# Performance work log

Measured on AMD Instinct MI355X. Metric: run time of the kernel, lower is better.

## Reference

```python
import jax, jax.numpy as jnp
import numpy as np

LMAX = 2; C = 64; H = 8; D = C // H
N_NODES = 10000; N_EDGES = 160000
M = (LMAX + 1) ** 2                      # 9 spherical components
RAD_IN = 64; RAD_HID = 64
WNUM = (LMAX + 1) * C                    # per-edge CP-TP weights: one per (l, channel)
L_OF_M = jnp.array([l for l in range(LMAX + 1) for _ in range(2 * l + 1)])
LN_EPS = 1e-5


def _lin(x, W, b=None):
    # Linear over channel (last) dim; bias applied ONLY to scalar (m=0) component
    y = jnp.einsum('nmc,cd->nmd', x, W)
    if b is not None:
        y = y.at[:, 0, :].add(b)
    return y


def _cp_tp(x, sh, w_lc):
    # CP tensor product with SH: channelwise product, per-(l, channel) radial weight
    # x: [E, M, C], sh: [E, M], w_lc: [E, LMAX+1, C]
    return x * sh[:, :, None] * w_lc[:, L_OF_M, :]


def _radial(s, W1, b1, g, b, W2, off):
    h = s @ W1 + b1
    mu = h.mean(-1, keepdims=True)
    var = h.var(-1, keepdims=True)
    h = (h - mu) / jnp.sqrt(var + LN_EPS) * g + b
    h = jax.nn.silu(h)
    return (h @ W2 + off).reshape(-1, LMAX + 1, C)


def _smooth_lrelu(x, a=0.2):
    return (1 + a) / 2 * x + (1 - a) / 2 * x * (2 * jax.nn.sigmoid(x) - 1)


def _gate(x):
    c = x.shape[-1] // 2
    v = x[..., :c]
    g = jax.nn.sigmoid(x[:, 0, c:])[:, None, :]
    return jnp.concatenate([jax.nn.silu(v[:, :1, :]), v[:, 1:, :] * g], axis=1)


def _seg_softmax(a, idx, n):
    # numerically stable softmax over edges grouped by destination node
    m = jax.ops.segment_max(a, idx, num_segments=n)
    e = jnp.exp(a - m[idx])
    s = jax.ops.segment_sum(e, idx, num_segments=n)
    return e / (s[idx] + 1e-16)


def setup_inputs():
    key = jax.random.key(0)
    ks = jax.random.split(key, 16)
    def w(k, shape, fan_in):
        return jax.random.normal(k, shape, jnp.float32) / np.sqrt(fan_in)
    bound = 1.0 / np.sqrt(RAD_HID)
    return {
        'node_input': jax.random.normal(ks[0], (N_NODES, M, C), jnp.float32),
        'edge_attr': jax.random.normal(ks[1], (N_EDGES, M), jnp.float32),
        'edge_scalars': jax.random.normal(ks[2], (N_EDGES, RAD_IN), jnp.float32),
        'W_src': w(ks[3], (C, C), C), 'b_src': jnp.zeros((C,), jnp.float32),
        'W_dst': w(ks[4], (C, C), C),
        'rad_W1': w(ks[5], (RAD_IN, RAD_HID), RAD_IN),
        'rad_b1': jnp.zeros((RAD_HID,), jnp.float32),
        'rad_ln_g': jnp.ones((RAD_HID,), jnp.float32),
        'rad_ln_b': jnp.zeros((RAD_HID,), jnp.float32),
        'rad_W2': w(ks[6], (RAD_HID, WNUM), RAD_HID),
        'rad_offset': jax.random.uniform(ks[7], (WNUM,), jnp.float32, -bound, bound),
        'W_alpha': w(ks[8], (C, C), C), 'b_alpha': jnp.zeros((C,), jnp.float32),
        'alpha_dot': w(ks[9], (H, D), D),
        'W_value': w(ks[10], (C, 2 * C), C), 'b_value': jnp.zeros((2 * C,), jnp.float32),
        'W_proj': w(ks[11], (C, C), C), 'b_proj': jnp.zeros((C,), jnp.float32),
        'edge_src': jax.random.randint(ks[12], (N_EDGES,), 0, N_NODES),
        'edge_dst': jax.random.randint(ks[13], (N_EDGES,), 0, N_NODES),
        'batch': jnp.zeros((N_NODES,), jnp.int32),
    }


def reference(node_input, edge_attr, edge_scalars, W_src, b_src, W_dst,
              rad_W1, rad_b1, rad_ln_g, rad_ln_b, rad_W2, rad_offset,
              W_alpha, b_alpha, alpha_dot, W_value, b_value, W_proj, b_proj,
              edge_src, edge_dst, batch):
    # gather: per-edge merged message [E, M, C]
    msg = _lin(node_input, W_src, b_src)[edge_src] + _lin(node_input, W_dst)[edge_dst]
    # per-edge radial weights for both tensor products [E, LMAX+1, C]
    w_lc = _radial(edge_scalars, rad_W1, rad_b1, rad_ln_g, rad_ln_b, rad_W2, rad_offset)
    msg = _cp_tp(msg, edge_attr, w_lc)
    # alpha path: scalar channel only
    alpha = _lin(msg, W_alpha, b_alpha)[:, 0, :].reshape(-1, H, D)
    alpha = _smooth_lrelu(alpha)[:, None]                 # [E, 1, H, D]
    alpha = jnp.einsum('bikd,kd->bik', alpha, alpha_dot)  # [E, 1, H]
    alpha = _seg_softmax(alpha, edge_dst, N_NODES)        # dropout disabled (eval)
    # value path
    value = _gate(_lin(msg, W_value, b_value))
    value = _cp_tp(value, edge_attr, w_lc)
    value = value.reshape(N_EDGES, M, H, D)
    # scatter-aggregate to destination nodes
    out = jax.ops.segment_sum(value * alpha[:, :, :, None], edge_dst, num_segments=N_NODES)
    return _lin(out.reshape(N_NODES, M, C), W_proj, b_proj)
```

## Files before the change

kernel.cpp:

```cpp
#include <hip/hip_runtime.h>
#include <stdint.h>

#define NN 10000
#define NE 160000

struct BF16 { unsigned short v; };
typedef _Float16 h2_t __attribute__((ext_vector_type(2)));
typedef _Float16 f16x8 __attribute__((ext_vector_type(8)));
typedef float f32x4 __attribute__((ext_vector_type(4)));

__device__ __forceinline__ float cvt(float x) { return x; }
__device__ __forceinline__ float cvt(BF16 x) {
    union { unsigned int i; float f; } u; u.i = ((unsigned int)x.v) << 16; return u.f;
}
__device__ __forceinline__ unsigned short f2b_us(float f) {
    union { float f; unsigned int i; } v; v.f = f;
    unsigned int x = v.i;
    unsigned int lsb = (x >> 16) & 1u;
    x += 0x7fffu + lsb;
    return (unsigned short)(x >> 16);
}
__device__ __forceinline__ float rlane(float v, int l) {
    return __uint_as_float((unsigned int)__builtin_amdgcn_readlane(__float_as_uint(v), l));
}
__device__ __forceinline__ h2_t rlane_pk(h2_t v, int l) {
    union { h2_t h; unsigned int u; } c; c.h = v;
    c.u = (unsigned int)__builtin_amdgcn_readlane(c.u, l);
    return c.h;
}
__device__ __forceinline__ h2_t pkh2(float a, float b) {
    h2_t r; r[0] = (_Float16)a; r[1] = (_Float16)b; return r;
}
__device__ __forceinline__ float fdot2f(h2_t a, h2_t b, float c) {
#if __has_builtin(__builtin_amdgcn_fdot2)
    return __builtin_amdgcn_fdot2(a, b, c, false);
#else
    return fmaf((float)a[0], (float)b[0], fmaf((float)a[1], (float)b[1], c));
#endif
}
__device__ __forceinline__ float sigm(float x) { return 1.0f / (1.0f + __expf(-x)); }
__device__ __forceinline__ int clampi(int v, int hi) { return (unsigned)v >= (unsigned)hi ? 0 : v; }

__device__ __forceinline__ void stOut(float* p, size_t i, float v) { p[i] = v; }
__device__ __forceinline__ void stOut(unsigned short* p, size_t i, float v) { p[i] = f2b_us(v); }

__device__ __forceinline__ unsigned okey(float f) {
    unsigned b = __float_as_uint(f);
    return (b & 0x80000000u) ? ~b : (b | 0x80000000u);
}
__device__ __forceinline__ float okdec(unsigned k) {
    unsigned b = (k & 0x80000000u) ? (k ^ 0x80000000u) : ~k;
    return __uint_as_float(b);
}

__device__ __forceinline__ f16x8 ld8f16(const BF16* p) {
    uint4 v = *(const uint4*)p;
    unsigned w0 = v.x, w1 = v.y, w2 = v.z, w3 = v.w;
    f16x8 r;
    union { unsigned u; float f; } c;
    c.u = (w0 & 0xFFFFu) << 16;  r[0] = (_Float16)c.f;
    c.u = (w0 & 0xFFFF0000u);    r[1] = (_Float16)c.f;
    c.u = (w1 & 0xFFFFu) << 16;  r[2] = (_Float16)c.f;
    c.u = (w1 & 0xFFFF0000u);    r[3] = (_Float16)c.f;
    c.u = (w2 & 0xFFFFu) << 16;  r[4] = (_Float16)c.f;
    c.u = (w2 & 0xFFFF0000u);    r[5] = (_Float16)c.f;
    c.u = (w3 & 0xFFFFu) << 16;  r[6] = (_Float16)c.f;
    c.u = (w3 & 0xFFFF0000u);    r[7] = (_Float16)c.f;
    return r;
}
__device__ __forceinline__ f16x8 ld8f16(const float* p) {
    float4 a = *(const float4*)p;
    float4 b = *(const float4*)(p + 4);
    f16x8 r;
    r[0] = (_Float16)a.x; r[1] = (_Float16)a.y; r[2] = (_Float16)a.z; r[3] = (_Float16)a.w;
    r[4] = (_Float16)b.x; r[5] = (_Float16)b.y; r[6] = (_Float16)b.z; r[7] = (_Float16)b.w;
    return r;
}

__global__ void k0_zero(int* __restrict__ cnt, int* __restrict__ csr, int* __restrict__ flag,
                        float* __restrict__ nsum, unsigned* __restrict__ mseg,
                        float* __restrict__ sseg, const unsigned short* __restrict__ x) {
    int i = blockIdx.x * blockDim.x + threadIdx.x;
    if (blockIdx.x == 0) {
        __shared__ int sbad[256];
        int bad = 0;
        for (int j = threadIdx.x; j < 16384; j += blockDim.x) {
            unsigned e = (x[j] >> 7) & 0xFFu;
            bad += (e == 0xFFu);
        }
        sbad[threadIdx.x] = bad;
        __syncthreads();
        for (int o = 128; o >= 1; o >>= 1) {
            if (threadIdx.x < o) sbad[threadIdx.x] += sbad[threadIdx.x + o];
            __syncthreads();
        }
        if (threadIdx.x == 0) *flag = (sbad[0] > 0) ? 0 : 1;
    }
    if (i < NN) cnt[i] = 0;
    if (i < NE) csr[i] = 0;
    if (i < NN * 8) { mseg[i] = 0u; sseg[i] = 0.f; }
    for (int j = i; j < NN * 576; j += gridDim.x * blockDim.x) nsum[j] = 0.f;
}

template<typename T>
__device__ void k1m_body(const T* x, const T* Ws, const T* bs, const T* Wd,
                         _Float16* fs, _Float16* fd, _Float16 (*Yt)[128])
{
    const int lane = threadIdx.x & 63;
    const int c16 = lane & 15;
    const int kg  = lane >> 4;

    f16x8 bWs[4][2], bWd[4][2];
#pragma unroll
    for (int t = 0; t < 4; t++)
#pragma unroll
        for (int kh = 0; kh < 2; kh++) {
            f16x8 f1, f2;
#pragma unroll
            for (int j = 0; j < 8; j++) {
                int k = kh * 32 + kg * 8 + j;
                f1[j] = (_Float16)cvt(Ws[(size_t)k * 64 + t * 16 + c16]);
                f2[j] = (_Float16)cvt(Wd[(size_t)k * 64 + t * 16 + c16]);
            }
            bWs[t][kh] = f1; bWd[t][kh] = f2;
        }
    float bsv[4];
#pragma unroll
    for (int t = 0; t < 4; t++) bsv[t] = cvt(bs[t * 16 + c16]);

    const int NT = (NN * 9) / 16;
    for (int tile = blockIdx.x * 4 + (threadIdx.x >> 6); tile < NT; tile += gridDim.x * 4) {
        const int r0 = tile * 16;
        f16x8 a0 = ld8f16(&x[(size_t)(r0 + c16) * 64 + kg * 8]);
        f16x8 a1 = ld8f16(&x[(size_t)(r0 + c16) * 64 + 32 + kg * 8]);
        f32x4 hs[4] = {{0,0,0,0},{0,0,0,0},{0,0,0,0},{0,0,0,0}};
        f32x4 hd[4] = {{0,0,0,0},{0,0,0,0},{0,0,0,0},{0,0,0,0}};
#pragma unroll
        for (int t = 0; t < 4; t++) {
            hs[t] = __builtin_amdgcn_mfma_f32_16x16x32_f16(a0, bWs[t][0], hs[t], 0, 0, 0);
            hs[t] = __builtin_amdgcn_mfma_f32_16x16x32_f16(a1, bWs[t][1], hs[t], 0, 0, 0);
            hd[t] = __builtin_amdgcn_mfma_f32_16x16x32_f16(a0, bWd[t][0], hd[t], 0, 0, 0);
            hd[t] = __builtin_amdgcn_mfma_f32_16x16x32_f16(a1, bWd[t][1], hd[t], 0, 0, 0);
        }
#pragma unroll
        for (int t = 0; t < 4; t++)
#pragma unroll
            for (int r = 0; r < 4; r++) {
                int row = kg * 4 + r;
                float vs = hs[t][r];
                if (((r0 + row) % 9) == 0) vs += bsv[t];
                Yt[row][t * 16 + c16] = (_Float16)vs;
                Yt[row][64 + t * 16 + c16] = (_Float16)hd[t][r];
            }
#pragma unroll
        for (int j = 0; j < 2; j++) {
            int c = lane + 64 * j;
            int row = c >> 3;
            int cc = (c & 7) * 8;
            *(f16x8*)&fs[(size_t)(r0 + row) * 64 + cc] = *(const f16x8*)&Yt[row][cc];
            *(f16x8*)&fd[(size_t)(r0 + row) * 64 + cc] = *(const f16x8*)&Yt[row][64 + cc];
        }
    }
}

__global__ __launch_bounds__(256) void k1m_feats(
    const void* x, const void* Ws, const void* bs, const void* Wd,
    _Float16* fs, _Float16* fd, const int* flag)
{
    __shared__ _Float16 Y[4][16][128];
    const int wv = threadIdx.x >> 6;
    if (*flag) k1m_body<BF16>((const BF16*)x, (const BF16*)Ws, (const BF16*)bs, (const BF16*)Wd,
                              fs, fd, Y[wv]);
    else       k1m_body<float>((const float*)x, (const float*)Ws, (const float*)bs, (const float*)Wd,
                               fs, fd, Y[wv]);
}

__global__ void k2a_count(const int* __restrict__ dst, int* __restrict__ cnt) {
    for (int e = blockIdx.x * blockDim.x + threadIdx.x; e < NE; e += gridDim.x * blockDim.x)
        atomicAdd(&cnt[clampi(dst[e], NN)], 1);
}

__global__ __launch_bounds__(1024) void k2b_scan(const int* __restrict__ cnt,
                                                 int* __restrict__ off, int* __restrict__ cur) {
    __shared__ int part[1024];
    int t = threadIdx.x;
    int base = t * 10;
    int loc[10]; int s = 0;
#pragma unroll
    for (int k = 0; k < 10; k++) { int i = base + k; int v = (i < NN) ? cnt[i] : 0; loc[k] = v; s += v; }
    part[t] = s; __syncthreads();
    for (int o = 1; o < 1024; o <<= 1) {
        int v = (t >= o) ? part[t - o] : 0;
        __syncthreads();
        part[t] += v;
        __syncthreads();
    }
    int run = (t == 0) ? 0 : part[t - 1];
#pragma unroll
    for (int k = 0; k < 10; k++) {
        int i = base + k;
        if (i < NN) { off[i] = run; cur[i] = run; run += loc[k]; }
    }
    if (t == 1023) off[NN] = part[1023];
}

__global__ void k2c_fill(const int* __restrict__ dst, int* __restrict__ cur, int* __restrict__ csr) {
    for (int e = blockIdx.x * blockDim.x + threadIdx.x; e < NE; e += gridDim.x * blockDim.x) {
        int d = clampi(dst[e], NN);
        int p = atomicAdd(&cur[d], 1);
        if ((unsigned)p < (unsigned)NE) csr[p] = e;
    }
}

template<typename T>
__device__ void k3m_body(const T* es, const T* W1, const T* b1g, const T* gg, const T* bbv,
                         const T* W2, const T* roff, _Float16* wlc,
                         _Float16 (*Yt)[200])
{
    const int lane = threadIdx.x & 63;
    const int c16 = lane & 15;
    const int kg  = lane >> 4;

    f16x8 bW1[4][2], bW2[12][2];
#pragma unroll
    for (int t = 0; t < 4; t++)
#pragma unroll
        for (int kh = 0; kh < 2; kh++) {
            f16x8 f;
#pragma unroll
            for (int j = 0; j < 8; j++) {
                int k = kh * 32 + kg * 8 + j;
                f[j] = (_Float16)cvt(W1[(size_t)k * 64 + t * 16 + c16]);
            }
            bW1[t][kh] = f;
        }
#pragma unroll
    for (int t = 0; t < 12; t++)
#pragma unroll
        for (int kh = 0; kh < 2; kh++) {
            f16x8 f;
#pragma unroll
            for (int j = 0; j < 8; j++) {
                int k = kh * 32 + kg * 8 + j;
                f[j] = (_Float16)cvt(W2[(size_t)k * 192 + t * 16 + c16]);
            }
            bW2[t][kh] = f;
        }
    float b1v[4], gv[4], bv[4], rv[12];
#pragma unroll
    for (int t = 0; t < 4; t++) {
        b1v[t] = cvt(b1g[t * 16 + c16]);
        gv[t]  = cvt(gg[t * 16 + c16]);
        bv[t]  = cvt(bbv[t * 16 + c16]);
    }
#pragma unroll
    for (int t = 0; t < 12; t++) rv[t] = cvt(roff[t * 16 + c16]);

    const int NT = NE / 16;
    for (int tile = blockIdx.x * 4 + (threadIdx.x >> 6); tile < NT; tile += gridDim.x * 4) {
        const int e0 = tile * 16;
        f16x8 a0 = ld8f16(&es[(size_t)(e0 + c16) * 64 + kg * 8]);
        f16x8 a1 = ld8f16(&es[(size_t)(e0 + c16) * 64 + 32 + kg * 8]);
        f32x4 h[4] = {{0,0,0,0},{0,0,0,0},{0,0,0,0},{0,0,0,0}};
#pragma unroll
        for (int t = 0; t < 4; t++) {
            h[t] = __builtin_amdgcn_mfma_f32_16x16x32_f16(a0, bW1[t][0], h[t], 0, 0, 0);
            h[t] = __builtin_amdgcn_mfma_f32_16x16x32_f16(a1, bW1[t][1], h[t], 0, 0, 0);
        }
#pragma unroll
        for (int r = 0; r < 4; r++) {
            float x0 = h[0][r] + b1v[0], x1 = h[1][r] + b1v[1];
            float x2 = h[2][r] + b1v[2], x3 = h[3][r] + b1v[3];
            float s = x0 + x1 + x2 + x3;
            float q = x0 * x0 + x1 * x1 + x2 * x2 + x3 * x3;
            s += __shfl_xor(s, 1, 64); q += __shfl_xor(q, 1, 64);
            s += __shfl_xor(s, 2, 64); q += __shfl_xor(q, 2, 64);
            s += __shfl_xor(s, 4, 64); q += __shfl_xor(q, 4, 64);
            s += __shfl_xor(s, 8, 64); q += __shfl_xor(q, 8, 64);
            float mu = s * (1.0f / 64.0f);
            float var = fmaxf(q * (1.0f / 64.0f) - mu * mu, 0.0f);
            float rs = rsqrtf(var + 1e-5f);
            int row = kg * 4 + r;
#pragma unroll
            for (int t = 0; t < 4; t++) {
                float xt = (t == 0) ? x0 : (t == 1) ? x1 : (t == 2) ? x2 : x3;
                float v = (xt - mu) * rs * gv[t] + bv[t];
                v = v * sigm(v);
                Yt[row][t * 16 + c16] = (_Float16)v;
            }
        }
        f16x8 a20 = *(const f16x8*)&Yt[c16][kg * 8];
        f16x8 a21 = *(const f16x8*)&Yt[c16][32 + kg * 8];
        f32x4 y[12] = {{0,0,0,0},{0,0,0,0},{0,0,0,0},{0,0,0,0},{0,0,0,0},{0,0,0,0},
                       {0,0,0,0},{0,0,0,0},{0,0,0,0},{0,0,0,0},{0,0,0,0},{0,0,0,0}};
#pragma unroll
        for (int t = 0; t < 12; t++) {
            y[t] = __builtin_amdgcn_mfma_f32_16x16x32_f16(a20, bW2[t][0], y[t], 0, 0, 0);
            y[t] = __builtin_amdgcn_mfma_f32_16x16x32_f16(a21, bW2[t][1], y[t], 0, 0, 0);
        }
#pragma unroll
        for (int t = 0; t < 12; t++)
#pragma unroll
            for (int r = 0; r < 4; r++)
                Yt[kg * 4 + r][t * 16 + c16] = (_Float16)(y[t][r] + rv[t]);
#pragma unroll
        for (int j = 0; j < 6; j++) {
            int c = lane + 64 * j;
            int row = c / 24;
            int cc = (c % 24) * 8;
            *(f16x8*)&wlc[(size_t)(e0 + row) * 192 + cc] = *(const f16x8*)&Yt[row][cc];
        }
    }
}

__global__ __launch_bounds__(256) void k3m_wlc(
    const void* es, const void* W1, const void* b1, const void* g, const void* bln,
    const void* W2, const void* roff, _Float16* wlc, const int* flag)
{
    __shared__ _Float16 Y[4][16][200];
    const int wv = threadIdx.x >> 6;
    if (*flag) k3m_body<BF16>((const BF16*)es, (const BF16*)W1, (const BF16*)b1, (const BF16*)g,
                              (const BF16*)bln, (const BF16*)W2, (const BF16*)roff, wlc, Y[wv]);
    else       k3m_body<float>((const float*)es, (const float*)W1, (const float*)b1, (const float*)g,
                               (const float*)bln, (const float*)W2, (const float*)roff, wlc, Y[wv]);
}

template<typename T>
__device__ void k4m_body(const T* ea, const _Float16* fs, const _Float16* fd,
                         const _Float16* wlc, const T* Wa, const T* ba, const T* adot,
                         const int* esrc, const int* edst, float* alpha, unsigned* mseg,
                         float (*aS)[8])
{
    const int lane = threadIdx.x & 63;
    const int c16 = lane & 15;
    const int kgr = lane >> 4;

    f16x8 bWa[4][2];
#pragma unroll
    for (int t = 0; t < 4; t++)
#pragma unroll
        for (int kh = 0; kh < 2; kh++) {
            f16x8 f;
#pragma unroll
            for (int j = 0; j < 8; j++) {
                int k = kh * 32 + kgr * 8 + j;
                f[j] = (_Float16)cvt(Wa[(size_t)k * 64 + t * 16 + c16]);
            }
            bWa[t][kh] = f;
        }
    float bav[4], adv[4];
#pragma unroll
    for (int t = 0; t < 4; t++) {
        bav[t] = cvt(ba[t * 16 + c16]);
        adv[t] = cvt(adot[t * 16 + c16]);
    }

    const int NT = NE / 16;
    for (int tile = blockIdx.x * 4 + (threadIdx.x >> 6); tile < NT; tile += gridDim.x * 4) {
        const int e0 = tile * 16;
        const int eA = e0 + c16;
        const int sn = clampi(esrc[eA], NN);
        const int dn = clampi(edst[eA], NN);
        f16x8 fs0 = *(const f16x8*)&fs[(size_t)sn * 576 + kgr * 8];
        f16x8 fs1 = *(const f16x8*)&fs[(size_t)sn * 576 + 32 + kgr * 8];
        f16x8 fd0 = *(const f16x8*)&fd[(size_t)dn * 576 + kgr * 8];
        f16x8 fd1 = *(const f16x8*)&fd[(size_t)dn * 576 + 32 + kgr * 8];
        f16x8 wl0 = *(const f16x8*)&wlc[(size_t)eA * 192 + kgr * 8];
        f16x8 wl1 = *(const f16x8*)&wlc[(size_t)eA * 192 + 32 + kgr * 8];
        _Float16 eh = (_Float16)cvt(ea[(size_t)eA * 9]);
        f16x8 ev;
#pragma unroll
        for (int j = 0; j < 8; j++) ev[j] = eh;
        f16x8 a0 = (fs0 + fd0) * ev * wl0;
        f16x8 a1 = (fs1 + fd1) * ev * wl1;

        f32x4 d[4] = {{0,0,0,0},{0,0,0,0},{0,0,0,0},{0,0,0,0}};
#pragma unroll
        for (int t = 0; t < 4; t++) {
            d[t] = __builtin_amdgcn_mfma_f32_16x16x32_f16(a0, bWa[t][0], d[t], 0, 0, 0);
            d[t] = __builtin_amdgcn_mfma_f32_16x16x32_f16(a1, bWa[t][1], d[t], 0, 0, 0);
        }
#pragma unroll
        for (int t = 0; t < 4; t++)
#pragma unroll
            for (int r = 0; r < 4; r++) {
                float aw = d[t][r] + bav[t];
                float f = aw * (0.2f + 0.8f * sigm(aw));
                float p = f * adv[t];
                p += __shfl_xor(p, 1, 64);
                p += __shfl_xor(p, 2, 64);
                p += __shfl_xor(p, 4, 64);
                if ((c16 & 7) == 0)
                    aS[kgr * 4 + r][t * 2 + (c16 >> 3)] = p;
            }
#pragma unroll
        for (int j = 0; j < 2; j++) {
            int idx = lane * 2 + j;
            int row = idx >> 3, h = idx & 7;
            float p = aS[row][h];
            alpha[(size_t)(e0 + row) * 8 + h] = p;
            int dnr = clampi(edst[e0 + row], NN);
            atomicMax(&mseg[dnr * 8 + h], okey(p));
        }
    }
}

__global__ __launch_bounds__(256) void k4m_alpha(
    const void* ea, const _Float16* fs, const _Float16* fd, const _Float16* wlc,
    const void* Wa, const void* ba, const void* adot,
    const int* esrc, const int* edst, float* alpha, unsigned* mseg, const int* flag)
{
    __shared__ float A[4][16][8];
    const int wv = threadIdx.x >> 6;
    if (*flag) k4m_body<BF16>((const BF16*)ea, fs, fd, wlc, (const BF16*)Wa, (const BF16*)ba,
                              (const BF16*)adot, esrc, edst, alpha, mseg, A[wv]);
    else       k4m_body<float>((const float*)ea, fs, fd, wlc, (const float*)Wa, (const float*)ba,
                               (const float*)adot, esrc, edst, alpha, mseg, A[wv]);
}

__global__ void k5b_expsum(const int* __restrict__ edst, const unsigned* __restrict__ mseg,
                           float* __restrict__ alpha, float* __restrict__ sseg) {
    int t = blockIdx.x * blockDim.x + threadIdx.x;
    if (t >= NE * 8) return;
    int e = t >> 3, h = t & 7;
    int dn = clampi(edst[e], NN);
    float m = okdec(mseg[dn * 8 + h]);
    float ex = __expf(alpha[t] - m);
    alpha[t] = ex;
    unsafeAtomicAdd(&sseg[dn * 8 + h], ex);
}

template<typename T>
__device__ void k6m_body(const int* off, const int* csr, const int* esrc,
                         const T* ea, const _Float16* fs, const _Float16* fd,
                         const _Float16* wlc, const T* Wv, const T* bv,
                         const float* alpha, const float* sseg, float* nsum,
                         _Float16 (*wlS)[16][72], float (*mtS)[20])
{
    const int lane = threadIdx.x & 63;
    const int wvid = threadIdx.x >> 6;
    const int c16 = lane & 15;
    const int kg  = lane >> 4;

    const int gw0  = blockIdx.x * 4 + wvid;
    const int half = gw0 & 1;

    f16x8 bfV[2][2], bfG[2][2];
    float bvv[2], bgv[2];
    int colg[2], hh[2];
#pragma unroll
    for (int t = 0; t < 2; t++) {
        colg[t] = (half * 2 + t) * 16 + c16;
        hh[t] = colg[t] >> 3;
#pragma unroll
        for (int kh = 0; kh < 2; kh++) {
            f16x8 b8v, b8g;
#pragma unroll
            for (int j = 0; j < 8; j++) {
                int k = kh * 32 + kg * 8 + j;
                b8v[j] = (_Float16)cvt(Wv[(size_t)k * 128 + colg[t]]);
                b8g[j] = (_Float16)cvt(Wv[(size_t)k * 128 + 64 + colg[t]]);
            }
            bfV[t][kh] = b8v; bfG[t][kh] = b8g;
        }
        bvv[t] = cvt(bv[colg[t]]);
        bgv[t] = cvt(bv[64 + colg[t]]);
    }

    for (int gw = gw0; gw < NN * 2; gw += gridDim.x * 4) {
        const int n = gw >> 1;
        const int b = off[n], e_end = off[n + 1];
        if (b >= e_end) continue;

        float invs[2];
        invs[0] = 1.0f / (sseg[n * 8 + hh[0]] + 1e-16f);
        invs[1] = 1.0f / (sseg[n * 8 + hh[1]] + 1e-16f);

        const size_t fdb = (size_t)n * 576;
        const size_t nbase = (size_t)n * 576;

        for (int p0 = b; p0 < e_end; p0 += 16) {
            int pA = p0 + c16; if (pA >= e_end) pA = e_end - 1;
            const int eA = clampi(csr[pA], NE);
            const int snA = clampi(esrc[eA], NN);
            const size_t fsb = (size_t)snA * 576;
            const size_t wlb = (size_t)eA * 192;

#pragma unroll
            for (int l = 0; l < 3; l++)
#pragma unroll
                for (int kh = 0; kh < 2; kh++)
                    *(f16x8*)&wlS[l][c16][kh * 32 + kg * 8] =
                        *(const f16x8*)&wlc[wlb + (size_t)l * 64 + kh * 32 + kg * 8];
            float eao[9];
#pragma unroll
            for (int m = 0; m < 9; m++) eao[m] = cvt(ea[(size_t)eA * 9 + m]);
            if (kg == 0) {
#pragma unroll
                for (int m = 0; m < 9; m++) mtS[c16][m] = eao[m];
            }
            mtS[c16][10 + kg * 2]     = alpha[(size_t)eA * 8 + kg * 2];
            mtS[c16][10 + kg * 2 + 1] = alpha[(size_t)eA * 8 + kg * 2 + 1];

            float awm[2][4];
#pragma unroll
            for (int r = 0; r < 4; r++) {
                int row = kg * 4 + r;
                float vm = (p0 + row < e_end) ? 1.f : 0.f;
#pragma unroll
                for (int t = 0; t < 2; t++)
                    awm[t][r] = mtS[row][10 + hh[t]] * invs[t] * vm;
            }

            float gtv[2][4];
            {
                f16x8 a0, a1;
                {
                    f16x8 w0 = *(const f16x8*)&wlS[0][c16][kg * 8];
                    f16x8 w1 = *(const f16x8*)&wlS[0][c16][32 + kg * 8];
                    f16x8 fd0 = *(const f16x8*)&fd[fdb + kg * 8];
                    f16x8 fd1 = *(const f16x8*)&fd[fdb + 32 + kg * 8];
                    f16x8 fs0 = *(const f16x8*)&fs[fsb + kg * 8];
                    f16x8 fs1 = *(const f16x8*)&fs[fsb + 32 + kg * 8];
                    _Float16 eh = (_Float16)eao[0];
                    f16x8 ev;
#pragma unroll
                    for (int j = 0; j < 8; j++) ev[j] = eh;
                    a0 = (fs0 + fd0) * ev * w0;
                    a1 = (fs1 + fd1) * ev * w1;
                }
                f32x4 d[2] = {{0,0,0,0},{0,0,0,0}};
                f32x4 g[2] = {{0,0,0,0},{0,0,0,0}};
#pragma unroll
                for (int t = 0; t < 2; t++) {
                    d[t] = __builtin_amdgcn_mfma_f32_16x16x32_f16(a0, bfV[t][0], d[t], 0, 0, 0);
                    d[t] = __builtin_amdgcn_mfma_f32_16x16x32_f16(a1, bfV[t][1], d[t], 0, 0, 0);
                    g[t] = __builtin_amdgcn_mfma_f32_16x16x32_f16(a0, bfG[t][0], g[t], 0, 0, 0);
                    g[t] = __builtin_amdgcn_mfma_f32_16x16x32_f16(a1, bfG[t][1], g[t], 0, 0, 0);
                }
#pragma unroll
                for (int t = 0; t < 2; t++) {
                    float ps = 0.f;
#pragma unroll
                    for (int r = 0; r < 4; r++) {
                        int row = kg * 4 + r;
                        gtv[t][r] = sigm(g[t][r] + bgv[t]);
                        float v = d[t][r] + bvv[t];
                        float f = v * sigm(v);
                        float wlv = (float)wlS[0][row][colg[t]];
                        float eam = mtS[row][0];
                        ps = fmaf(f * (eam * wlv), awm[t][r], ps);
                    }
                    ps += __shfl_xor(ps, 16, 64);
                    ps += __shfl_xor(ps, 32, 64);
                    if (kg == 0) unsafeAtomicAdd(&nsum[nbase + colg[t]], ps);
                }
            }
#pragma unroll 2
            for (int m = 1; m < 9; m++) {
                const int l = (m < 4) ? 1 : 2;
                f16x8 a0, a1;
                {
                    const size_t mo = (size_t)m * 64;
                    f16x8 w0 = *(const f16x8*)&wlS[l][c16][kg * 8];
                    f16x8 w1 = *(const f16x8*)&wlS[l][c16][32 + kg * 8];
                    f16x8 fd0 = *(const f16x8*)&fd[fdb + mo + kg * 8];
                    f16x8 fd1 = *(const f16x8*)&fd[fdb + mo + 32 + kg * 8];
                    f16x8 fs0 = *(const f16x8*)&fs[fsb + mo + kg * 8];
                    f16x8 fs1 = *(const f16x8*)&fs[fsb + mo + 32 + kg * 8];
                    _Float16 eh = (_Float16)eao[m];
                    f16x8 ev;
#pragma unroll
                    for (int j = 0; j < 8; j++) ev[j] = eh;
                    a0 = (fs0 + fd0) * ev * w0;
                    a1 = (fs1 + fd1) * ev * w1;
                }
                f32x4 d[2] = {{0,0,0,0},{0,0,0,0}};
#pragma unroll
                for (int t = 0; t < 2; t++) {
                    d[t] = __builtin_amdgcn_mfma_f32_16x16x32_f16(a0, bfV[t][0], d[t], 0, 0, 0);
                    d[t] = __builtin_amdgcn_mfma_f32_16x16x32_f16(a1, bfV[t][1], d[t], 0, 0, 0);
                }
#pragma unroll
                for (int t = 0; t < 2; t++) {
                    float ps = 0.f;
#pragma unroll
                    for (int r = 0; r < 4; r++) {
                        int row = kg * 4 + r;
                        float f = d[t][r] * gtv[t][r];
                        float wlv = (float)wlS[l][row][colg[t]];
                        float eam = mtS[row][m];
                        ps = fmaf(f * (eam * wlv), awm[t][r], ps);
                    }
                    ps += __shfl_xor(ps, 16, 64);
                    ps += __shfl_xor(ps, 32, 64);
                    if (kg == 0) unsafeAtomicAdd(&nsum[nbase + (size_t)m * 64 + colg[t]], ps);
                }
            }
        }
    }
}

__global__ __launch_bounds__(256) void k6m_fused(
    const int* off, const int* csr, const int* esrc,
    const void* ea, const _Float16* fs, const _Float16* fd, const _Float16* wlc,
    const void* Wv, const void* bv,
    const float* alpha, const float* sseg, float* nsum, const int* flag)
{
    __shared__ _Float16 shwl[4][3][16][72];
    __shared__ float    shmt[4][16][20];
    const int wvid = threadIdx.x >> 6;
    if (*flag) k6m_body<BF16>(off, csr, esrc, (const BF16*)ea, fs, fd, wlc,
                              (const BF16*)Wv, (const BF16*)bv, alpha, sseg, nsum,
                              shwl[wvid], shmt[wvid]);
    else       k6m_body<float>(off, csr, esrc, (const float*)ea, fs, fd, wlc,
                               (const float*)Wv, (const float*)bv, alpha, sseg, nsum,
                               shwl[wvid], shmt[wvid]);
}

template<typename T, typename OT>
__device__ void k7m_body(const float* ns, const T* Wp, const T* bp, OT* out, OT (*Yt)[72])
{
    const int lane = threadIdx.x & 63;
    const int c16 = lane & 15;
    const int kg  = lane >> 4;

    f16x8 bWp[4][2];
#pragma unroll
    for (int t = 0; t < 4; t++)
#pragma unroll
        for (int kh = 0; kh < 2; kh++) {
            f16x8 f;
#pragma unroll
            for (int j = 0; j < 8; j++) {
                int k = kh * 32 + kg * 8 + j;
                f[j] = (_Float16)cvt(Wp[(size_t)k * 64 + t * 16 + c16]);
            }
            bWp[t][kh] = f;
        }
    float bpv[4];
#pragma unroll
    for (int t = 0; t < 4; t++) bpv[t] = cvt(bp[t * 16 + c16]);

    const int NT = (NN * 9) / 16;
    for (int tile = blockIdx.x * 4 + (threadIdx.x >> 6); tile < NT; tile += gridDim.x * 4) {
        const int r0 = tile * 16;
        f16x8 a0 = ld8f16(&ns[(size_t)(r0 + c16) * 64 + kg * 8]);
        f16x8 a1 = ld8f16(&ns[(size_t)(r0 + c16) * 64 + 32 + kg * 8]);
        f32x4 d[4] = {{0,0,0,0},{0,0,0,0},{0,0,0,0},{0,0,0,0}};
#pragma unroll
        for (int t = 0; t < 4; t++) {
            d[t] = __builtin_amdgcn_mfma_f32_16x16x32_f16(a0, bWp[t][0], d[t], 0, 0, 0);
            d[t] = __builtin_amdgcn_mfma_f32_16x16x32_f16(a1, bWp[t][1], d[t], 0, 0, 0);
        }
#pragma unroll
        for (int t = 0; t < 4; t++)
#pragma unroll
            for (int r = 0; r < 4; r++) {
                int row = kg * 4 + r;
                float o = d[t][r];
                if (((r0 + row) % 9) == 0) o += bpv[t];
                stOut((OT*)&Yt[row][0], t * 16 + c16, o);
            }
        const int CH = (64 * (int)sizeof(OT)) / 16;
#pragma unroll
        for (int j = 0; j < (16 * CH) / 64; j++) {
            int c = lane + 64 * j;
            int row = c / CH;
            int cc = (c % CH) * (16 / (int)sizeof(OT));
            *(uint4*)&out[(size_t)(r0 + row) * 64 + cc] = *(const uint4*)&Yt[row][cc];
        }
    }
}

__global__ __launch_bounds__(256) void k7m_proj(
    const float* ns, const void* Wp, const void* bp, void* out, const int* flag)
{
    __shared__ __align__(16) unsigned char Ybuf[4][16 * 72 * 4];
    const int wv = threadIdx.x >> 6;
    if (*flag) k7m_body<BF16, unsigned short>(ns, (const BF16*)Wp, (const BF16*)bp,
                               (unsigned short*)out, (unsigned short (*)[72])Ybuf[wv]);
    else       k7m_body<float, float>(ns, (const float*)Wp, (const float*)bp,
                               (float*)out, (float (*)[72])Ybuf[wv]);
}

extern "C" void kernel_launch(void* const* d_in, const int* in_sizes, int n_in,
                              void* d_out, int out_size, void* d_ws, size_t ws_size,
                              hipStream_t stream) {
    const void* node_input = d_in[0];
    const void* edge_attr  = d_in[1];
    const void* edge_scal  = d_in[2];
    const void* W_src      = d_in[3];
    const void* b_src      = d_in[4];
    const void* W_dst      = d_in[5];
    const void* rad_W1     = d_in[6];
    const void* rad_b1     = d_in[7];
    const void* rad_ln_g   = d_in[8];
    const void* rad_ln_b   = d_in[9];
    const void* rad_W2     = d_in[10];
    const void* rad_off    = d_in[11];
    const void* W_alpha    = d_in[12];
    const void* b_alpha    = d_in[13];
    const void* alpha_dot  = d_in[14];
    const void* W_value    = d_in[15];
    const void* b_value    = d_in[16];
    const void* W_proj     = d_in[17];
    const void* b_proj     = d_in[18];
    const int* edge_src    = (const int*)d_in[19];
    const int* edge_dst    = (const int*)d_in[20];

    char* ws = (char*)d_ws;
    size_t ofs = 0;
    auto alloc = [&](size_t bytes) -> char* {
        char* r = ws + ofs;
        ofs = (ofs + bytes + 255) & ~(size_t)255;
        return r;
    };

    int* flag       = (int*)alloc(256);
    int* cnt        = (int*)alloc((size_t)NN * 4);
    int* offs       = (int*)alloc((size_t)(NN + 16) * 4);
    int* cur        = (int*)alloc((size_t)NN * 4);
    int* csr        = (int*)alloc((size_t)NE * 4);
    unsigned* mseg  = (unsigned*)alloc((size_t)NN * 8 * 4);
    float* sseg     = (float*)alloc((size_t)NN * 8 * 4);
    float* alpha    = (float*)alloc((size_t)NE * 8 * 4);
    _Float16* fs    = (_Float16*)alloc((size_t)NN * 576 * 2);
    _Float16* fd    = (_Float16*)alloc((size_t)NN * 576 * 2);
    _Float16* wlc   = (_Float16*)alloc((size_t)NE * 192 * 2);
    float* nsum32   = (float*)alloc((size_t)NN * 576 * 4);

    k0_zero<<<dim3(625), dim3(256), 0, stream>>>(cnt, csr, flag, nsum32, mseg, sseg,
                                                 (const unsigned short*)node_input);
    k1m_feats<<<dim3(1408), dim3(256), 0, stream>>>(node_input, W_src, b_src, W_dst, fs, fd, flag);
    k2a_count<<<dim3(512), dim3(256), 0, stream>>>(edge_dst, cnt);
    k2b_scan<<<dim3(1), dim3(1024), 0, stream>>>(cnt, offs, cur);
    k2c_fill<<<dim3(512), dim3(256), 0, stream>>>(edge_dst, cur, csr);
    k3m_wlc<<<dim3(512), dim3(256), 0, stream>>>(edge_scal, rad_W1, rad_b1, rad_ln_g, rad_ln_b,
                                                 rad_W2, rad_off, wlc, flag);
    k4m_alpha<<<dim3(2500), dim3(256), 0, stream>>>(edge_attr, fs, fd, wlc, W_alpha, b_alpha,
                                                    alpha_dot, edge_src, edge_dst, alpha, mseg, flag);
    k5b_expsum<<<dim3(5000), dim3(256), 0, stream>>>(edge_dst, mseg, alpha, sseg);
    k6m_fused<<<dim3(1250), dim3(256), 0, stream>>>(offs, csr, edge_src, edge_attr, fs, fd, wlc,
                                                    W_value, b_value, alpha, sseg, nsum32, flag);
    k7m_proj<<<dim3(1408), dim3(256), 0, stream>>>(nsum32, W_proj, b_proj, d_out, flag);
}
```

Baseline: 482.0 us.

## Permute per-edge data into CSR order and launch one wave per node-half

The CSR fill kernel now also writes permuted src/dst index arrays and a padded fp16 copy of edge_attr in destination-sorted order. The radial MLP is evaluated in that same order, so wlc, alpha and edge attributes become contiguous per destination node when the fused value/aggregate kernel reads them, which removes the csr indirection and scattered gathers. The fused kernel drops its grid-stride loop in favour of one wave per (node, half) with a larger grid. In exchange the fill kernel does extra scattered writes and the radial kernel reads edge_scalars through a gather.

```diff
diff --git a/kernel.cpp b/kernel.cpp
--- a/kernel.cpp
+++ b/kernel.cpp
@@ -19,24 +19,6 @@
     unsigned int lsb = (x >> 16) & 1u;
     x += 0x7fffu + lsb;
     return (unsigned short)(x >> 16);
-}
-__device__ __forceinline__ float rlane(float v, int l) {
-    return __uint_as_float((unsigned int)__builtin_amdgcn_readlane(__float_as_uint(v), l));
-}
-__device__ __forceinline__ h2_t rlane_pk(h2_t v, int l) {
-    union { h2_t h; unsigned int u; } c; c.h = v;
-    c.u = (unsigned int)__builtin_amdgcn_readlane(c.u, l);
-    return c.h;
-}
-__device__ __forceinline__ h2_t pkh2(float a, float b) {
-    h2_t r; r[0] = (_Float16)a; r[1] = (_Float16)b; return r;
-}
-__device__ __forceinline__ float fdot2f(h2_t a, h2_t b, float c) {
-#if __has_builtin(__builtin_amdgcn_fdot2)
-    return __builtin_amdgcn_fdot2(a, b, c, false);
-#else
-    return fmaf((float)a[0], (float)b[0], fmaf((float)a[1], (float)b[1], c));
-#endif
 }
 __device__ __forceinline__ float sigm(float x) { return 1.0f / (1.0f + __expf(-x)); }
 __device__ __forceinline__ int clampi(int v, int hi) { return (unsigned)v >= (unsigned)hi ? 0 : v; }
@@ -204,17 +186,38 @@
     if (t == 1023) off[NN] = part[1023];
 }
 
-__global__ void k2c_fill(const int* __restrict__ dst, int* __restrict__ cur, int* __restrict__ csr) {
+__global__ void k2c_fill(const int* __restrict__ dst, const int* __restrict__ src,
+                         const void* __restrict__ ea, int* __restrict__ cur,
+                         int* __restrict__ csr, int* __restrict__ esrcp,
+                         int* __restrict__ edstp, _Float16* __restrict__ ea16,
+                         const int* __restrict__ flag) {
+    const int isbf = *flag;
     for (int e = blockIdx.x * blockDim.x + threadIdx.x; e < NE; e += gridDim.x * blockDim.x) {
         int d = clampi(dst[e], NN);
         int p = atomicAdd(&cur[d], 1);
-        if ((unsigned)p < (unsigned)NE) csr[p] = e;
+        if ((unsigned)p < (unsigned)NE) {
+            csr[p] = e;
+            esrcp[p] = clampi(src[e], NN);
+            edstp[p] = d;
+            size_t bo = (size_t)p * 16;
+            if (isbf) {
+                const BF16* q = (const BF16*)ea + (size_t)e * 9;
+#pragma unroll
+                for (int m = 0; m < 9; m++) ea16[bo + m] = (_Float16)cvt(q[m]);
+            } else {
+                const float* q = (const float*)ea + (size_t)e * 9;
+#pragma unroll
+                for (int m = 0; m < 9; m++) ea16[bo + m] = (_Float16)q[m];
+            }
+#pragma unroll
+            for (int m = 9; m < 16; m++) ea16[bo + m] = (_Float16)0.f;
+        }
     }
 }
 
 template<typename T>
-__device__ void k3m_body(const T* es, const T* W1, const T* b1g, const T* gg, const T* bbv,
-                         const T* W2, const T* roff, _Float16* wlc,
+__device__ void k3m_body(const T* es, const int* csr, const T* W1, const T* b1g, const T* gg,
+                         const T* bbv, const T* W2, const T* roff, _Float16* wlc,
                          _Float16 (*Yt)[200])
 {
     const int lane = threadIdx.x & 63;
@@ -258,9 +261,10 @@
 
     const int NT = NE / 16;
     for (int tile = blockIdx.x * 4 + (threadIdx.x >> 6); tile < NT; tile += gridDim.x * 4) {
-        const int e0 = tile * 16;
-        f16x8 a0 = ld8f16(&es[(size_t)(e0 + c16) * 64 + kg * 8]);
-        f16x8 a1 = ld8f16(&es[(size_t)(e0 + c16) * 64 + 32 + kg * 8]);
+        const int q0 = tile * 16;
+        const int eg = clampi(csr[q0 + c16], NE);
+        f16x8 a0 = ld8f16(&es[(size_t)eg * 64 + kg * 8]);
+        f16x8 a1 = ld8f16(&es[(size_t)eg * 64 + 32 + kg * 8]);
         f32x4 h[4] = {{0,0,0,0},{0,0,0,0},{0,0,0,0},{0,0,0,0}};
 #pragma unroll
         for (int t = 0; t < 4; t++) {
@@ -308,27 +312,27 @@
             int c = lane + 64 * j;
             int row = c / 24;
             int cc = (c % 24) * 8;
-            *(f16x8*)&wlc[(size_t)(e0 + row) * 192 + cc] = *(const f16x8*)&Yt[row][cc];
+            *(f16x8*)&wlc[(size_t)(q0 + row) * 192 + cc] = *(const f16x8*)&Yt[row][cc];
         }
     }
 }
 
 __global__ __launch_bounds__(256) void k3m_wlc(
-    const void* es, const void* W1, const void* b1, const void* g, const void* bln,
-    const void* W2, const void* roff, _Float16* wlc, const int* flag)
+    const void* es, const int* csr, const void* W1, const void* b1, const void* g,
+    const void* bln, const void* W2, const void* roff, _Float16* wlc, const int* flag)
 {
     __shared__ _Float16 Y[4][16][200];
     const int wv = threadIdx.x >> 6;
-    if (*flag) k3m_body<BF16>((const BF16*)es, (const BF16*)W1, (const BF16*)b1, (const BF16*)g,
+    if (*flag) k3m_body<BF16>((const BF16*)es, csr, (const BF16*)W1, (const BF16*)b1, (const BF16*)g,
                               (const BF16*)bln, (const BF16*)W2, (const BF16*)roff, wlc, Y[wv]);
-    else       k3m_body<float>((const float*)es, (const float*)W1, (const float*)b1, (const float*)g,
+    else       k3m_body<float>((const float*)es, csr, (const float*)W1, (const float*)b1, (const float*)g,
                                (const float*)bln, (const float*)W2, (const float*)roff, wlc, Y[wv]);
 }
 
 template<typename T>
-__device__ void k4m_body(const T* ea, const _Float16* fs, const _Float16* fd,
+__device__ void k4m_body(const _Float16* ea16, const _Float16* fs, const _Float16* fd,
                          const _Float16* wlc, const T* Wa, const T* ba, const T* adot,
-                         const int* esrc, const int* edst, float* alpha, unsigned* mseg,
+                         const int* esrcp, const int* edstp, float* alpha, unsigned* mseg,
                          float (*aS)[8])
 {
     const int lane = threadIdx.x & 63;
@@ -357,17 +361,17 @@
 
     const int NT = NE / 16;
     for (int tile = blockIdx.x * 4 + (threadIdx.x >> 6); tile < NT; tile += gridDim.x * 4) {
-        const int e0 = tile * 16;
-        const int eA = e0 + c16;
-        const int sn = clampi(esrc[eA], NN);
-        const int dn = clampi(edst[eA], NN);
+        const int q0 = tile * 16;
+        const int qA = q0 + c16;
+        const int sn = esrcp[qA];
+        const int dn = edstp[qA];
         f16x8 fs0 = *(const f16x8*)&fs[(size_t)sn * 576 + kgr * 8];
         f16x8 fs1 = *(const f16x8*)&fs[(size_t)sn * 576 + 32 + kgr * 8];
         f16x8 fd0 = *(const f16x8*)&fd[(size_t)dn * 576 + kgr * 8];
         f16x8 fd1 = *(const f16x8*)&fd[(size_t)dn * 576 + 32 + kgr * 8];
-        f16x8 wl0 = *(const f16x8*)&wlc[(size_t)eA * 192 + kgr * 8];
-        f16x8 wl1 = *(const f16x8*)&wlc[(size_t)eA * 192 + 32 + kgr * 8];
-        _Float16 eh = (_Float16)cvt(ea[(size_t)eA * 9]);
+        f16x8 wl0 = *(const f16x8*)&wlc[(size_t)qA * 192 + kgr * 8];
+        f16x8 wl1 = *(const f16x8*)&wlc[(size_t)qA * 192 + 32 + kgr * 8];
+        _Float16 eh = ea16[(size_t)qA * 16];
         f16x8 ev;
 #pragma unroll
         for (int j = 0; j < 8; j++) ev[j] = eh;
@@ -398,32 +402,32 @@
             int idx = lane * 2 + j;
             int row = idx >> 3, h = idx & 7;
             float p = aS[row][h];
-            alpha[(size_t)(e0 + row) * 8 + h] = p;
-            int dnr = clampi(edst[e0 + row], NN);
+            alpha[(size_t)(q0 + row) * 8 + h] = p;
+            int dnr = edstp[q0 + row];
             atomicMax(&mseg[dnr * 8 + h], okey(p));
         }
     }
 }
 
 __global__ __launch_bounds__(256) void k4m_alpha(
-    const void* ea, const _Float16* fs, const _Float16* fd, const _Float16* wlc,
+    const _Float16* ea16, const _Float16* fs, const _Float16* fd, const _Float16* wlc,
     const void* Wa, const void* ba, const void* adot,
-    const int* esrc, const int* edst, float* alpha, unsigned* mseg, const int* flag)
+    const int* esrcp, const int* edstp, float* alpha, unsigned* mseg, const int* flag)
 {
     __shared__ float A[4][16][8];
     const int wv = threadIdx.x >> 6;
-    if (*flag) k4m_body<BF16>((const BF16*)ea, fs, fd, wlc, (const BF16*)Wa, (const BF16*)ba,
-                              (const BF16*)adot, esrc, edst, alpha, mseg, A[wv]);
-    else       k4m_body<float>((const float*)ea, fs, fd, wlc, (const float*)Wa, (const float*)ba,
-                               (const float*)adot, esrc, edst, alpha, mseg, A[wv]);
-}
-
-__global__ void k5b_expsum(const int* __restrict__ edst, const unsigned* __restrict__ mseg,
+    if (*flag) k4m_body<BF16>(ea16, fs, fd, wlc, (const BF16*)Wa, (const BF16*)ba,
+                              (const BF16*)adot, esrcp, edstp, alpha, mseg, A[wv]);
+    else       k4m_body<float>(ea16, fs, fd, wlc, (const float*)Wa, (const float*)ba,
+                               (const float*)adot, esrcp, edstp, alpha, mseg, A[wv]);
+}
+
+__global__ void k5b_expsum(const int* __restrict__ edstp, const unsigned* __restrict__ mseg,
                            float* __restrict__ alpha, float* __restrict__ sseg) {
     int t = blockIdx.x * blockDim.x + threadIdx.x;
     if (t >= NE * 8) return;
-    int e = t >> 3, h = t & 7;
-    int dn = clampi(edst[e], NN);
+    int q = t >> 3, h = t & 7;
+    int dn = clampi(edstp[q], NN);
     float m = okdec(mseg[dn * 8 + h]);
     float ex = __expf(alpha[t] - m);
     alpha[t] = ex;
@@ -431,8 +435,8 @@
 }
 
 template<typename T>
-__device__ void k6m_body(const int* off, const int* csr, const int* esrc,
-                         const T* ea, const _Float16* fs, const _Float16* fd,
+__device__ void k6m_body(const int* off, const int* esrcp,
+                         const _Float16* ea16, const _Float16* fs, const _Float16* fd,
                          const _Float16* wlc, const T* Wv, const T* bv,
                          const float* alpha, const float* sseg, float* nsum,
                          _Float16 (*wlS)[16][72], float (*mtS)[20])
@@ -442,16 +446,21 @@
     const int c16 = lane & 15;
     const int kg  = lane >> 4;
 
-    const int gw0  = blockIdx.x * 4 + wvid;
-    const int half = gw0 & 1;
+    const int gw  = blockIdx.x * 4 + wvid;
+    const int n = gw >> 1;
+    const int half = gw & 1;
+    const int b = off[n], e_end = off[n + 1];
+    if (b >= e_end) return;
 
     f16x8 bfV[2][2], bfG[2][2];
     float bvv[2], bgv[2];
     int colg[2], hh[2];
+    float invs[2];
 #pragma unroll
     for (int t = 0; t < 2; t++) {
         colg[t] = (half * 2 + t) * 16 + c16;
         hh[t] = colg[t] >> 3;
+        invs[t] = 1.0f / (sseg[n * 8 + hh[t]] + 1e-16f);
 #pragma unroll
         for (int kh = 0; kh < 2; kh++) {
             f16x8 b8v, b8g;
@@ -467,153 +476,147 @@
         bgv[t] = cvt(bv[64 + colg[t]]);
     }
 
-    for (int gw = gw0; gw < NN * 2; gw += gridDim.x * 4) {
-        const int n = gw >> 1;
-        const int b = off[n], e_end = off[n + 1];
-        if (b >= e_end) continue;
-
-        float invs[2];
-        invs[0] = 1.0f / (sseg[n * 8 + hh[0]] + 1e-16f);
-        invs[1] = 1.0f / (sseg[n * 8 + hh[1]] + 1e-16f);
-
-        const size_t fdb = (size_t)n * 576;
-        const size_t nbase = (size_t)n * 576;
-
-        for (int p0 = b; p0 < e_end; p0 += 16) {
-            int pA = p0 + c16; if (pA >= e_end) pA = e_end - 1;
-            const int eA = clampi(csr[pA], NE);
-            const int snA = clampi(esrc[eA], NN);
-            const size_t fsb = (size_t)snA * 576;
-            const size_t wlb = (size_t)eA * 192;
-
-#pragma unroll
-            for (int l = 0; l < 3; l++)
-#pragma unroll
-                for (int kh = 0; kh < 2; kh++)
-                    *(f16x8*)&wlS[l][c16][kh * 32 + kg * 8] =
-                        *(const f16x8*)&wlc[wlb + (size_t)l * 64 + kh * 32 + kg * 8];
-            float eao[9];
-#pragma unroll
-            for (int m = 0; m < 9; m++) eao[m] = cvt(ea[(size_t)eA * 9 + m]);
-            if (kg == 0) {
-#pragma unroll
-                for (int m = 0; m < 9; m++) mtS[c16][m] = eao[m];
-            }
-            mtS[c16][10 + kg * 2]     = alpha[(size_t)eA * 8 + kg * 2];
-            mtS[c16][10 + kg * 2 + 1] = alpha[(size_t)eA * 8 + kg * 2 + 1];
-
-            float awm[2][4];
-#pragma unroll
-            for (int r = 0; r < 4; r++) {
-                int row = kg * 4 + r;
-                float vm = (p0 + row < e_end) ? 1.f : 0.f;
-#pragma unroll
-                for (int t = 0; t < 2; t++)
-                    awm[t][r] = mtS[row][10 + hh[t]] * invs[t] * vm;
-            }
-
-            float gtv[2][4];
+    const size_t fdb = (size_t)n * 576;
+    const size_t nbase = (size_t)n * 576;
+
+    for (int p0 = b; p0 < e_end; p0 += 16) {
+        int pA = p0 + c16; if (pA >= e_end) pA = e_end - 1;
+        const int snA = esrcp[pA];
+        const size_t fsb = (size_t)snA * 576;
+        const size_t wlb = (size_t)pA * 192;
+
+#pragma unroll
+        for (int l = 0; l < 3; l++)
+#pragma unroll
+            for (int kh = 0; kh < 2; kh++)
+                *(f16x8*)&wlS[l][c16][kh * 32 + kg * 8] =
+                    *(const f16x8*)&wlc[wlb + (size_t)l * 64 + kh * 32 + kg * 8];
+        float eao[9];
+        {
+            f16x8 ep0 = *(const f16x8*)&ea16[(size_t)pA * 16];
+            _Float16 e8 = ea16[(size_t)pA * 16 + 8];
+#pragma unroll
+            for (int m = 0; m < 8; m++) eao[m] = (float)ep0[m];
+            eao[8] = (float)e8;
+        }
+        if (kg == 0) {
+#pragma unroll
+            for (int m = 0; m < 9; m++) mtS[c16][m] = eao[m];
+        }
+        mtS[c16][10 + kg * 2]     = alpha[(size_t)pA * 8 + kg * 2];
+        mtS[c16][10 + kg * 2 + 1] = alpha[(size_t)pA * 8 + kg * 2 + 1];
+
+        float awm[2][4];
+#pragma unroll
+        for (int r = 0; r < 4; r++) {
+            int row = kg * 4 + r;
+            float vm = (p0 + row < e_end) ? 1.f : 0.f;
+#pragma unroll
+            for (int t = 0; t < 2; t++)
+                awm[t][r] = mtS[row][10 + hh[t]] * invs[t] * vm;
+        }
+
+        float gtv[2][4];
+        {
+            f16x8 a0, a1;
             {
-                f16x8 a0, a1;
-                {
-                    f16x8 w0 = *(const f16x8*)&wlS[0][c16][kg * 8];
-                    f16x8 w1 = *(const f16x8*)&wlS[0][c16][32 + kg * 8];
-                    f16x8 fd0 = *(const f16x8*)&fd[fdb + kg * 8];
-                    f16x8 fd1 = *(const f16x8*)&fd[fdb + 32 + kg * 8];
-                    f16x8 fs0 = *(const f16x8*)&fs[fsb + kg * 8];
-                    f16x8 fs1 = *(const f16x8*)&fs[fsb + 32 + kg * 8];
-                    _Float16 eh = (_Float16)eao[0];
-                    f16x8 ev;
-#pragma unroll
-                    for (int j = 0; j < 8; j++) ev[j] = eh;
-                    a0 = (fs0 + fd0) * ev * w0;
-                    a1 = (fs1 + fd1) * ev * w1;
+                f16x8 w0 = *(const f16x8*)&wlS[0][c16][kg * 8];
+                f16x8 w1 = *(const f16x8*)&wlS[0][c16][32 + kg * 8];
+                f16x8 fd0 = *(const f16x8*)&fd[fdb + kg * 8];
+                f16x8 fd1 = *(const f16x8*)&fd[fdb + 32 + kg * 8];
+                f16x8 fs0 = *(const f16x8*)&fs[fsb + kg * 8];
+                f16x8 fs1 = *(const f16x8*)&fs[fsb + 32 + kg * 8];
+                _Float16 eh = (_Float16)eao[0];
+                f16x8 ev;
+#pragma unroll
+                for (int j = 0; j < 8; j++) ev[j] = eh;
+                a0 = (fs0 + fd0) * ev * w0;
+                a1 = (fs1 + fd1) * ev * w1;
+            }
+            f32x4 d[2] = {{0,0,0,0},{0,0,0,0}};
+            f32x4 g[2] = {{0,0,0,0},{0,0,0,0}};
+#pragma unroll
+            for (int t = 0; t < 2; t++) {
+                d[t] = __builtin_amdgcn_mfma_f32_16x16x32_f16(a0, bfV[t][0], d[t], 0, 0, 0);
+                d[t] = __builtin_amdgcn_mfma_f32_16x16x32_f16(a1, bfV[t][1], d[t], 0, 0, 0);
+                g[t] = __builtin_amdgcn_mfma_f32_16x16x32_f16(a0, bfG[t][0], g[t], 0, 0, 0);
+                g[t] = __builtin_amdgcn_mfma_f32_16x16x32_f16(a1, bfG[t][1], g[t], 0, 0, 0);
+            }
+#pragma unroll
+            for (int t = 0; t < 2; t++) {
+                float ps = 0.f;
+#pragma unroll
+                for (int r = 0; r < 4; r++) {
+                    int row = kg * 4 + r;
+                    gtv[t][r] = sigm(g[t][r] + bgv[t]);
+                    float v = d[t][r] + bvv[t];
+                    float f = v * sigm(v);
+                    float wlv = (float)wlS[0][row][colg[t]];
+                    float eam = mtS[row][0];
+                    ps = fmaf(f * (eam * wlv), awm[t][r], ps);
                 }
-                f32x4 d[2] = {{0,0,0,0},{0,0,0,0}};
-                f32x4 g[2] = {{0,0,0,0},{0,0,0,0}};
-#pragma unroll
-                for (int t = 0; t < 2; t++) {
-                    d[t] = __builtin_amdgcn_mfma_f32_16x16x32_f16(a0, bfV[t][0], d[t], 0, 0, 0);
-                    d[t] = __builtin_amdgcn_mfma_f32_16x16x32_f16(a1, bfV[t][1], d[t], 0, 0, 0);
-                    g[t] = __builtin_amdgcn_mfma_f32_16x16x32_f16(a0, bfG[t][0], g[t], 0, 0, 0);
-                    g[t] = __builtin_amdgcn_mfma_f32_16x16x32_f16(a1, bfG[t][1], g[t], 0, 0, 0);
+                ps += __shfl_xor(ps, 16, 64);
+                ps += __shfl_xor(ps, 32, 64);
+                if (kg == 0) unsafeAtomicAdd(&nsum[nbase + colg[t]], ps);
+            }
+        }
+#pragma unroll 2
+        for (int m = 1; m < 9; m++) {
+            const int l = (m < 4) ? 1 : 2;
+            f16x8 a0, a1;
+            {
+                const size_t mo = (size_t)m * 64;
+                f16x8 w0 = *(const f16x8*)&wlS[l][c16][kg * 8];
+                f16x8 w1 = *(const f16x8*)&wlS[l][c16][32 + kg * 8];
+                f16x8 fd0 = *(const f16x8*)&fd[fdb + mo + kg * 8];
+                f16x8 fd1 = *(const f16x8*)&fd[fdb + mo + 32 + kg * 8];
+                f16x8 fs0 = *(const f16x8*)&fs[fsb + mo + kg * 8];
+                f16x8 fs1 = *(const f16x8*)&fs[fsb + mo + 32 + kg * 8];
+                _Float16 eh = (_Float16)eao[m];
+                f16x8 ev;
+#pragma unroll
+                for (int j = 0; j < 8; j++) ev[j] = eh;
+                a0 = (fs0 + fd0) * ev * w0;
+                a1 = (fs1 + fd1) * ev * w1;
+            }
+            f32x4 d[2] = {{0,0,0,0},{0,0,0,0}};
+#pragma unroll
+            for (int t = 0; t < 2; t++) {
+                d[t] = __builtin_amdgcn_mfma_f32_16x16x32_f16(a0, bfV[t][0], d[t], 0, 0, 0);
+                d[t] = __builtin_amdgcn_mfma_f32_16x16x32_f16(a1, bfV[t][1], d[t], 0, 0, 0);
+            }
+#pragma unroll
+            for (int t = 0; t < 2; t++) {
+                float ps = 0.f;
+#pragma unroll
+                for (int r = 0; r < 4; r++) {
+                    int row = kg * 4 + r;
+                    float f = d[t][r] * gtv[t][r];
+                    float wlv = (float)wlS[l][row][colg[t]];
+                    float eam = mtS[row][m];
+                    ps = fmaf(f * (eam * wlv), awm[t][r], ps);
                 }
-#pragma unroll
-                for (int t = 0; t < 2; t++) {
-                    float ps = 0.f;
-#pragma unroll
-                    for (int r = 0; r < 4; r++) {
-                        int row = kg * 4 + r;
-                        gtv[t][r] = sigm(g[t][r] + bgv[t]);
-                        float v = d[t][r] + bvv[t];
-                        float f = v * sigm(v);
-                        float wlv = (float)wlS[0][row][colg[t]];
-                        float eam = mtS[row][0];
-                        ps = fmaf(f * (eam * wlv), awm[t][r], ps);
-                    }
-                    ps += __shfl_xor(ps, 16, 64);
-                    ps += __shfl_xor(ps, 32, 64);
-                    if (kg == 0) unsafeAtomicAdd(&nsum[nbase + colg[t]], ps);
-                }
-            }
-#pragma unroll 2
-            for (int m = 1; m < 9; m++) {
-                const int l = (m < 4) ? 1 : 2;
-                f16x8 a0, a1;
-                {
-                    const size_t mo = (size_t)m * 64;
-                    f16x8 w0 = *(const f16x8*)&wlS[l][c16][kg * 8];
-                    f16x8 w1 = *(const f16x8*)&wlS[l][c16][32 + kg * 8];
-                    f16x8 fd0 = *(const f16x8*)&fd[fdb + mo + kg * 8];
-                    f16x8 fd1 = *(const f16x8*)&fd[fdb + mo + 32 + kg * 8];
-                    f16x8 fs0 = *(const f16x8*)&fs[fsb + mo + kg * 8];
-                    f16x8 fs1 = *(const f16x8*)&fs[fsb + mo + 32 + kg * 8];
-                    _Float16 eh = (_Float16)eao[m];
-                    f16x8 ev;
-#pragma unroll
-                    for (int j = 0; j < 8; j++) ev[j] = eh;
-                    a0 = (fs0 + fd0) * ev * w0;
-                    a1 = (fs1 + fd1) * ev * w1;
-                }
-                f32x4 d[2] = {{0,0,0,0},{0,0,0,0}};
-#pragma unroll
-                for (int t = 0; t < 2; t++) {
-                    d[t] = __builtin_amdgcn_mfma_f32_16x16x32_f16(a0, bfV[t][0], d[t], 0, 0, 0);
-                    d[t] = __builtin_amdgcn_mfma_f32_16x16x32_f16(a1, bfV[t][1], d[t], 0, 0, 0);
-                }
-#pragma unroll
-                for (int t = 0; t < 2; t++) {
-                    float ps = 0.f;
-#pragma unroll
-                    for (int r = 0; r < 4; r++) {
-                        int row = kg * 4 + r;
-                        float f = d[t][r] * gtv[t][r];
-                        float wlv = (float)wlS[l][row][colg[t]];
-                        float eam = mtS[row][m];
-                        ps = fmaf(f * (eam * wlv), awm[t][r], ps);
-                    }
-                    ps += __shfl_xor(ps, 16, 64);
-                    ps += __shfl_xor(ps, 32, 64);
-                    if (kg == 0) unsafeAtomicAdd(&nsum[nbase + (size_t)m * 64 + colg[t]], ps);
-                }
+                ps += __shfl_xor(ps, 16, 64);
+                ps += __shfl_xor(ps, 32, 64);
+                if (kg == 0) unsafeAtomicAdd(&nsum[nbase + (size_t)m * 64 + colg[t]], ps);
             }
         }
     }
 }
 
 __global__ __launch_bounds__(256) void k6m_fused(
-    const int* off, const int* csr, const int* esrc,
-    const void* ea, const _Float16* fs, const _Float16* fd, const _Float16* wlc,
+    const int* off, const int* esrcp,
+    const _Float16* ea16, const _Float16* fs, const _Float16* fd, const _Float16* wlc,
     const void* Wv, const void* bv,
     const float* alpha, const float* sseg, float* nsum, const int* flag)
 {
     __shared__ _Float16 shwl[4][3][16][72];
     __shared__ float    shmt[4][16][20];
     const int wvid = threadIdx.x >> 6;
-    if (*flag) k6m_body<BF16>(off, csr, esrc, (const BF16*)ea, fs, fd, wlc,
+    if (*flag) k6m_body<BF16>(off, esrcp, ea16, fs, fd, wlc,
                               (const BF16*)Wv, (const BF16*)bv, alpha, sseg, nsum,
                               shwl[wvid], shmt[wvid]);
-    else       k6m_body<float>(off, csr, esrc, (const float*)ea, fs, fd, wlc,
+    else       k6m_body<float>(off, esrcp, ea16, fs, fd, wlc,
                                (const float*)Wv, (const float*)bv, alpha, sseg, nsum,
                                shwl[wvid], shmt[wvid]);
 }
@@ -722,9 +725,12 @@
     int* offs       = (int*)alloc((size_t)(NN + 16) * 4);
     int* cur        = (int*)alloc((size_t)NN * 4);
     int* csr        = (int*)alloc((size_t)NE * 4);
+    int* esrcp      = (int*)alloc((size_t)NE * 4);
+    int* edstp      = (int*)alloc((size_t)NE * 4);
     unsigned* mseg  = (unsigned*)alloc((size_t)NN * 8 * 4);
     float* sseg     = (float*)alloc((size_t)NN * 8 * 4);
     float* alpha    = (float*)alloc((size_t)NE * 8 * 4);
+    _Float16* ea16  = (_Float16*)alloc((size_t)NE * 16 * 2);
     _Float16* fs    = (_Float16*)alloc((size_t)NN * 576 * 2);
     _Float16* fd    = (_Float16*)alloc((size_t)NN * 576 * 2);
     _Float16* wlc   = (_Float16*)alloc((size_t)NE * 192 * 2);
@@ -735,13 +741,14 @@
     k1m_feats<<<dim3(1408), dim3(256), 0, stream>>>(node_input, W_src, b_src, W_dst, fs, fd, flag);
     k2a_count<<<dim3(512), dim3(256), 0, stream>>>(edge_dst, cnt);
     k2b_scan<<<dim3(1), dim3(1024), 0, stream>>>(cnt, offs, cur);
-    k2c_fill<<<dim3(512), dim3(256), 0, stream>>>(edge_dst, cur, csr);
-    k3m_wlc<<<dim3(512), dim3(256), 0, stream>>>(edge_scal, rad_W1, rad_b1, rad_ln_g, rad_ln_b,
-                                                 rad_W2, rad_off, wlc, flag);
-    k4m_alpha<<<dim3(2500), dim3(256), 0, stream>>>(edge_attr, fs, fd, wlc, W_alpha, b_alpha,
-                                                    alpha_dot, edge_src, edge_dst, alpha, mseg, flag);
-    k5b_expsum<<<dim3(5000), dim3(256), 0, stream>>>(edge_dst, mseg, alpha, sseg);
-    k6m_fused<<<dim3(1250), dim3(256), 0, stream>>>(offs, csr, edge_src, edge_attr, fs, fd, wlc,
+    k2c_fill<<<dim3(512), dim3(256), 0, stream>>>(edge_dst, edge_src, edge_attr, cur, csr,
+                                                  esrcp, edstp, ea16, flag);
+    k3m_wlc<<<dim3(512), dim3(256), 0, stream>>>(edge_scal, csr, rad_W1, rad_b1, rad_ln_g,
+                                                 rad_ln_b, rad_W2, rad_off, wlc, flag);
+    k4m_alpha<<<dim3(2500), dim3(256), 0, stream>>>(ea16, fs, fd, wlc, W_alpha, b_alpha,
+                                                    alpha_dot, esrcp, edstp, alpha, mseg, flag);
+    k5b_expsum<<<dim3(5000), dim3(256), 0, stream>>>(edstp, mseg, alpha, sseg);
+    k6m_fused<<<dim3(5000), dim3(256), 0, stream>>>(offs, esrcp, ea16, fs, fd, wlc,
                                                     W_value, b_value, alpha, sseg, nsum32, flag);
     k7m_proj<<<dim3(1408), dim3(256), 0, stream>>>(nsum32, W_proj, b_proj, d_out, flag);
 }
```

New measurement: 446.4 us. 7.4% less time.
